# Kernel optimization log

Hardware: AMD Instinct MI355X
Metric: run time of the kernel (lower is better)

Reference implementation:

```python
import jax, jax.numpy as jnp
import numpy as np

EPS = 1e-5
DEPTH = 3
NQ = 12


def _bn(x, g, b):
    # BatchNorm1d in training mode: batch statistics, biased variance
    mu = x.mean(0)
    var = x.var(0)
    return (x - mu) / jnp.sqrt(var + EPS) * g + b


def _ln(x, g, b):
    mu = x.mean(-1, keepdims=True)
    var = x.var(-1, keepdims=True)
    return (x - mu) / jnp.sqrt(var + EPS) * g + b


def _apply_1q(s, U, q):
    # s: [B, 2^NQ] complex; U: [2,2] (shared) or [B,2,2] (per-sample); qubit q = q-th MSB
    B = s.shape[0]
    s = s.reshape(B, 2 ** q, 2, -1)
    sub = 'ij,bajc->baic' if U.ndim == 2 else 'bij,bajc->baic'
    return jnp.einsum(sub, U, s).reshape(B, -1)


def _apply_cry(s, theta, c):
    # controlled-Ry(theta): control qubit c, target qubit c+1 (adjacent)
    B = s.shape[0]
    s = s.reshape(B, 2 ** c, 2, 2, -1)
    co = jnp.cos(theta / 2).astype(s.dtype)
    si = jnp.sin(theta / 2).astype(s.dtype)
    s1 = s[:, :, 1]  # control = |1> block
    new1 = jnp.stack([co * s1[:, :, 0] - si * s1[:, :, 1],
                      si * s1[:, :, 0] + co * s1[:, :, 1]], axis=2)
    s = jnp.concatenate([s[:, :, :1], new1[:, :, None]], axis=2)
    return s.reshape(B, -1)


def _measure(s):
    # P(qubit q measures |1>) for each qubit
    p = jnp.abs(s) ** 2  # [B, 2^NQ]
    B = p.shape[0]
    probs = [p.reshape(B, 2 ** q, 2, -1).sum(axis=(1, 3))[:, 1] for q in range(NQ)]
    return jnp.stack(probs, axis=1)  # [B, NQ]


def _rot_mats(rot):
    # fused Rz(rz) @ Ry(ry) @ Rx(rx) for each (depth, qubit) -> [DEPTH, NQ, 2, 2]
    hx, hy, hz = rot[..., 0] / 2, rot[..., 1] / 2, rot[..., 2] / 2
    cx, sx = jnp.cos(hx), jnp.sin(hx)
    Rx = jnp.stack([jnp.stack([cx + 0j, -1j * sx], -1),
                    jnp.stack([-1j * sx, cx + 0j], -1)], -2)
    cy, sy = jnp.cos(hy), jnp.sin(hy)
    Ry = jnp.stack([jnp.stack([cy, -sy], -1),
                    jnp.stack([sy, cy], -1)], -2).astype(jnp.complex64)
    ez = jnp.exp(-1j * hz)
    z0 = jnp.zeros_like(ez)
    Rz = jnp.stack([jnp.stack([ez, z0], -1),
                    jnp.stack([z0, jnp.conj(ez)], -1)], -2)
    return jnp.einsum('...ij,...jk,...kl->...il', Rz, Ry, Rx).astype(jnp.complex64)


def _quantum_layer(x, We, be, gi, bi, rot, ent, Wd, bd, go, bo):
    e = jnp.tanh(_bn(x @ We.T + be, gi, bi))  # [B, NQ]
    nrm = jnp.linalg.norm(e, axis=1, keepdims=True)
    a = jnp.where(nrm > 0, e / nrm, e)        # per-sample L2-normalized amplitudes
    B = x.shape[0]
    s = jnp.zeros((B, 2 ** NQ), jnp.complex64).at[:, 0].set(1.0)
    # amplitude encoding: Ry(2*arcsin(|a|)) then phase pi (sign) if a<0 -> diag(1,-1)@Ry
    ang = 2.0 * jnp.arcsin(jnp.clip(jnp.abs(a), 0.0, 1.0))
    c, si = jnp.cos(ang / 2), jnp.sin(ang / 2)
    sg = jnp.where(a < 0, -1.0, 1.0)
    for q in range(NQ):
        U = jnp.stack([jnp.stack([c[:, q], -si[:, q]], -1),
                       jnp.stack([sg[:, q] * si[:, q], sg[:, q] * c[:, q]], -1)],
                      -2).astype(jnp.complex64)  # [B,2,2]
        s = _apply_1q(s, U, q)
    # parameterized circuit: per-qubit fused Rz.Ry.Rx, then nearest-neighbor CRy chain
    U = _rot_mats(rot)
    for d in range(DEPTH):
        for q in range(NQ):
            s = _apply_1q(s, U[d, q], q)
        for i in range(NQ - 1):
            s = _apply_cry(s, ent[d, i], i)
    m = _measure(s)
    return _bn(m @ Wd.T + bd, go, bo)


def setup_inputs() -> dict:
    key = jax.random.key(0)
    ks = jax.random.split(key, 16)
    B, IN, H1, H2, H3, OUT = 512, 512, 512, 512, 1024, 256

    def lin(k, o, i):
        k1, k2 = jax.random.split(k)
        lim = 1.0 / np.sqrt(i)
        return (jax.random.uniform(k1, (o, i), jnp.float32, -lim, lim),
                jax.random.uniform(k2, (o,), jnp.float32, -lim, lim))

    qWe0, qbe0 = lin(ks[1], NQ, IN)
    qWd0, qbd0 = lin(ks[2], H1, NQ)
    qWe1, qbe1 = lin(ks[3], NQ, H1)
    qWd1, qbd1 = lin(ks[4], H2, NQ)
    W2, b2 = lin(ks[5], H3, H2)
    Wo, bo = lin(ks[6], OUT, H3)
    return {
        'x': jax.random.normal(ks[0], (B, IN), jnp.float32),
        'qWe0': qWe0, 'qbe0': qbe0,
        'qgi0': jnp.ones(NQ), 'qbi0': jnp.zeros(NQ),
        'rot0': 0.1 * jax.random.normal(ks[7], (DEPTH, NQ, 3), jnp.float32),
        'ent0': 0.1 * jax.random.normal(ks[8], (DEPTH, NQ - 1), jnp.float32),
        'qWd0': qWd0, 'qbd0': qbd0,
        'qgo0': jnp.ones(H1), 'qbo0': jnp.zeros(H1),
        'qWe1': qWe1, 'qbe1': qbe1,
        'qgi1': jnp.ones(NQ), 'qbi1': jnp.zeros(NQ),
        'rot1': 0.1 * jax.random.normal(ks[9], (DEPTH, NQ, 3), jnp.float32),
        'ent1': 0.1 * jax.random.normal(ks[10], (DEPTH, NQ - 1), jnp.float32),
        'qWd1': qWd1, 'qbd1': qbd1,
        'qgo1': jnp.ones(H2), 'qbo1': jnp.zeros(H2),
        'W2': W2, 'b2': b2, 'ln2g': jnp.ones(H3), 'ln2b': jnp.zeros(H3),
        'Wo': Wo, 'bo': bo, 'lnog': jnp.ones(OUT), 'lnob': jnp.zeros(OUT),
    }


def reference(x, qWe0, qbe0, qgi0, qbi0, rot0, ent0, qWd0, qbd0, qgo0, qbo0,
              qWe1, qbe1, qgi1, qbi1, rot1, ent1, qWd1, qbd1, qgo1, qbo1,
              W2, b2, ln2g, ln2b, Wo, bo, lnog, lnob):
    h = _quantum_layer(x, qWe0, qbe0, qgi0, qbi0, rot0, ent0, qWd0, qbd0, qgo0, qbo0)
    h = _quantum_layer(h, qWe1, qbe1, qgi1, qbi1, rot1, ent1, qWd1, qbd1, qgo1, qbo1)
    h = jax.nn.relu(_ln(h @ W2.T + b2, ln2g, ln2b))  # classical block (dropout = identity, eval)
    return _ln(h @ Wo.T + bo, lnog, lnob)
```

## Files before the change

kernel.cpp:

```cpp
#include <hip/hip_runtime.h>
#include <math.h>

#define EPS   1e-5f
#define NQ    12
#define DEPTH 3
#define BATCH 512
#define DIM   4096

__device__ inline float2 cmul(float2 a, float2 b) {
    return make_float2(a.x*b.x - a.y*b.y, a.x*b.y + a.y*b.x);
}
__device__ inline float2 cmac2(float2 ua, float2 s, float2 ub, float2 p) {
    return make_float2(ua.x*s.x - ua.y*s.y + ub.x*p.x - ub.y*p.y,
                       ua.x*s.y + ua.y*s.x + ub.x*p.y + ub.y*p.x);
}

__device__ inline int swz(int a) { return a ^ ((a >> 4) & 15); }

template<int L> __device__ inline int ampl(int tid, int k) {
    if constexpr (L == 1) return (k << 8) | tid;
    else if constexpr (L == 2) return ((tid & 0xE0) << 4) | (k << 5) | (tid & 0x1F);
    else if constexpr (L == 3) return ((tid & 0xFC) << 4) | (k << 2) | (tid & 3);
    else return (tid << 4) | k;
}

template<int F, int T>
__device__ inline void remap(float2* amp, float2* lds2, int tid) {
    #pragma unroll
    for (int k = 0; k < 16; ++k) lds2[swz(ampl<F>(tid, k))] = amp[k];
    __syncthreads();
    #pragma unroll
    for (int k = 0; k < 16; ++k) amp[k] = lds2[swz(ampl<T>(tid, k))];
    __syncthreads();
}

template<int BP>
__device__ inline void one_q(float2* amp, float2 u00, float2 u01, float2 u10, float2 u11) {
    #pragma unroll
    for (int g = 0; g < 8; ++g) {
        const int j0 = ((g >> BP) << (BP+1)) | (g & ((1<<BP)-1));
        const int j1 = j0 | (1 << BP);
        float2 a0 = amp[j0], a1 = amp[j1];
        amp[j0] = cmac2(u00, a0, u01, a1);
        amp[j1] = cmac2(u10, a0, u11, a1);
    }
}

template<int CB, int TB>
__device__ inline void cry_rr(float2* amp, float co, float si) {
    #pragma unroll
    for (int m = 0; m < 16; ++m) {
        if (((m >> CB) & 1) && !((m >> TB) & 1)) {
            const int j1 = m | (1 << TB);
            float2 a0 = amp[m], a1 = amp[j1];
            amp[m]  = make_float2(co*a0.x - si*a1.x, co*a0.y - si*a1.y);
            amp[j1] = make_float2(si*a0.x + co*a1.x, si*a0.y + co*a1.y);
        }
    }
}

__device__ void qsim_core(float2* amp, float2* lds2, float* redm,
                          const float2* Uc, const float2* Cc,
                          int tid, int b, float* mout) {
    for (int d = 0; d < DEPTH; ++d) {
        const float2* Ud = Uc + d*NQ*4;
        const float2* Cd = Cc + d*(NQ-1);
        if (d > 0) {
            remap<4,1>(amp, lds2, tid);
            one_q<3>(amp, Ud[0],  Ud[1],  Ud[2],  Ud[3]);
            one_q<2>(amp, Ud[4],  Ud[5],  Ud[6],  Ud[7]);
            one_q<1>(amp, Ud[8],  Ud[9],  Ud[10], Ud[11]);
            one_q<0>(amp, Ud[12], Ud[13], Ud[14], Ud[15]);
        }
        cry_rr<3,2>(amp, Cd[0].x, Cd[0].y);
        cry_rr<2,1>(amp, Cd[1].x, Cd[1].y);
        cry_rr<1,0>(amp, Cd[2].x, Cd[2].y);
        remap<1,2>(amp, lds2, tid);
        if (d > 0) {
            one_q<2>(amp, Ud[16], Ud[17], Ud[18], Ud[19]);
            one_q<1>(amp, Ud[20], Ud[21], Ud[22], Ud[23]);
            one_q<0>(amp, Ud[24], Ud[25], Ud[26], Ud[27]);
        }
        cry_rr<3,2>(amp, Cd[3].x, Cd[3].y);
        cry_rr<2,1>(amp, Cd[4].x, Cd[4].y);
        cry_rr<1,0>(amp, Cd[5].x, Cd[5].y);
        remap<2,3>(amp, lds2, tid);
        if (d > 0) {
            one_q<2>(amp, Ud[28], Ud[29], Ud[30], Ud[31]);
            one_q<1>(amp, Ud[32], Ud[33], Ud[34], Ud[35]);
            one_q<0>(amp, Ud[36], Ud[37], Ud[38], Ud[39]);
        }
        cry_rr<3,2>(amp, Cd[6].x, Cd[6].y);
        cry_rr<2,1>(amp, Cd[7].x, Cd[7].y);
        cry_rr<1,0>(amp, Cd[8].x, Cd[8].y);
        remap<3,4>(amp, lds2, tid);
        if (d > 0) {
            one_q<1>(amp, Ud[40], Ud[41], Ud[42], Ud[43]);
            one_q<0>(amp, Ud[44], Ud[45], Ud[46], Ud[47]);
        }
        cry_rr<2,1>(amp, Cd[9].x,  Cd[9].y);
        cry_rr<1,0>(amp, Cd[10].x, Cd[10].y);
    }
    float msum = 0.f, p8 = 0.f, p9 = 0.f, p10 = 0.f, p11 = 0.f;
    #pragma unroll
    for (int k = 0; k < 16; ++k) {
        float m = amp[k].x*amp[k].x + amp[k].y*amp[k].y;
        msum += m;
        if (k & 8) p8  += m;
        if (k & 4) p9  += m;
        if (k & 2) p10 += m;
        if (k & 1) p11 += m;
    }
    int lane = tid & 63, wave = tid >> 6;
    #pragma unroll
    for (int q = 0; q < NQ; ++q) {
        float v;
        if (q < 8)        v = ((tid >> (7-q)) & 1) ? msum : 0.f;
        else if (q == 8)  v = p8;
        else if (q == 9)  v = p9;
        else if (q == 10) v = p10;
        else              v = p11;
        #pragma unroll
        for (int off = 32; off; off >>= 1) v += __shfl_xor(v, off);
        if (lane == 0) redm[q*4 + wave] = v;
    }
    __syncthreads();
    if (tid < NQ)
        mout[b*NQ + tid] = redm[tid*4] + redm[tid*4+1] + redm[tid*4+2] + redm[tid*4+3];
}

__device__ void qsim_init(float2* amp, const float* a, const float2* Uc, int tid) {
    float2 v0[NQ], v1[NQ];
    #pragma unroll
    for (int q = 0; q < NQ; ++q) {
        float sv = fminf(fabsf(a[q]), 1.f);
        float c  = sqrtf(fmaxf(1.f - sv*sv, 0.f));
        float ss = (a[q] < 0.f) ? -sv : sv;
        const float2* U = Uc + q*4;
        v0[q] = make_float2(U[0].x*c + U[1].x*ss, U[0].y*c + U[1].y*ss);
        v1[q] = make_float2(U[2].x*c + U[3].x*ss, U[2].y*c + U[3].y*ss);
    }
    float2 common = make_float2(1.f, 0.f);
    #pragma unroll
    for (int bb = 0; bb < 8; ++bb)
        common = cmul(common, ((tid >> bb) & 1) ? v1[11-bb] : v0[11-bb]);
    amp[0] = common;
    #pragma unroll
    for (int m = 0; m < 4; ++m) {
        const int q = 3 - m;
        #pragma unroll
        for (int k = 0; k < (1<<m); ++k) {
            amp[k | (1<<m)] = cmul(amp[k], v1[q]);
            amp[k]          = cmul(amp[k], v0[q]);
        }
    }
}

__device__ void consts_body(int t,
        const float* rot0, const float* ent0, const float* rot1, const float* ent1,
        float2* Uc, float2* Cc) {
    if (t < 72) {
        int layer = t / 36, rem = t % 36, d = rem / 12, q = rem % 12;
        const float* rot = layer ? rot1 : rot0;
        float hx = 0.5f * rot[(d*NQ + q)*3 + 0];
        float hy = 0.5f * rot[(d*NQ + q)*3 + 1];
        float hz = 0.5f * rot[(d*NQ + q)*3 + 2];
        float cx = cosf(hx), sx = sinf(hx);
        float cy = cosf(hy), sy = sinf(hy);
        float2 m00 = make_float2( cy*cx,  sy*sx);
        float2 m01 = make_float2(-sy*cx, -cy*sx);
        float2 m10 = make_float2( sy*cx, -cy*sx);
        float2 m11 = make_float2( cy*cx, -sy*sx);
        float2 ez  = make_float2(cosf(hz), -sinf(hz));
        float2 ezc = make_float2(ez.x, -ez.y);
        float2* U = Uc + t*4;
        U[0] = cmul(ez,  m00);
        U[1] = cmul(ez,  m01);
        U[2] = cmul(ezc, m10);
        U[3] = cmul(ezc, m11);
    } else if (t < 72 + 66) {
        int idx = t - 72, layer = idx / 33, rem = idx % 33;
        const float* ent = layer ? ent1 : ent0;
        float th = 0.5f * ent[rem];
        Cc[idx] = make_float2(cosf(th), sinf(th));
    }
}

__global__ __launch_bounds__(256) void encode0_consts_kernel(
        const float* __restrict__ X, const float* __restrict__ We,
        const float* __restrict__ be, float* __restrict__ Yraw,
        const float* __restrict__ rot0, const float* __restrict__ ent0,
        const float* __restrict__ rot1, const float* __restrict__ ent1,
        float2* __restrict__ Uc, float2* __restrict__ Cc) {
    int tid = threadIdx.x;
    if (blockIdx.x == 128) {
        consts_body(tid, rot0, ent0, rot1, ent1, Uc, Cc);
        return;
    }
    __shared__ float w[NQ][512];
    {
        const float4* src = (const float4*)We;
        float4* dst = (float4*)&w[0][0];
        #pragma unroll
        for (int i = tid; i < NQ*128; i += 256) dst[i] = src[i];
    }
    __syncthreads();
    int wave = tid >> 6, lane = tid & 63;
    int b = blockIdx.x * 4 + wave;
    const float4* xr = (const float4*)(X + (size_t)b * 512);
    float acc[NQ] = {};
    #pragma unroll
    for (int j = 0; j < 2; ++j) {
        float4 xv = xr[lane + 64*j];
        #pragma unroll
        for (int q = 0; q < NQ; ++q) {
            float4 wv = ((const float4*)&w[q][0])[lane + 64*j];
            acc[q] += xv.x*wv.x + xv.y*wv.y + xv.z*wv.z + xv.w*wv.w;
        }
    }
    #pragma unroll
    for (int q = 0; q < NQ; ++q) {
        float v = acc[q];
        #pragma unroll
        for (int off = 32; off; off >>= 1) v += __shfl_xor(v, off);
        if (lane == q) Yraw[b*NQ + q] = v + be[q];
    }
}

__global__ __launch_bounds__(256) void qsim_fused_kernel(
        const float* __restrict__ Yraw, const float* __restrict__ gi,
        const float* __restrict__ bi, const float2* __restrict__ UcAll,
        const float2* __restrict__ CcAll, int layer,
        float* __restrict__ mout, float* __restrict__ zeroY) {
    int blk = blockIdx.x, tid = threadIdx.x;
    const float2* UcL = UcAll + layer * DEPTH * NQ * 4;
    const float2* CcL = CcAll + layer * DEPTH * (NQ - 1);
    __shared__ float2 lds2[DIM];
    __shared__ float sred[96];
    if (zeroY && tid < NQ) zeroY[blk*NQ + tid] = 0.f;
    float sum[NQ] = {}, sq[NQ] = {};
    const float4* Y4 = (const float4*)Yraw;
    #pragma unroll
    for (int j = 0; j < 6; ++j) {
        float4 v = Y4[tid*6 + j];
        int q0 = (j*4) % 12;
        sum[q0+0]+=v.x; sq[q0+0]+=v.x*v.x;
        sum[q0+1]+=v.y; sq[q0+1]+=v.y*v.y;
        sum[q0+2]+=v.z; sq[q0+2]+=v.z*v.z;
        sum[q0+3]+=v.w; sq[q0+3]+=v.w*v.w;
    }
    int lane = tid & 63, wave = tid >> 6;
    #pragma unroll
    for (int q = 0; q < NQ; ++q) {
        #pragma unroll
        for (int off = 32; off; off >>= 1) {
            sum[q] += __shfl_xor(sum[q], off);
            sq[q]  += __shfl_xor(sq[q],  off);
        }
    }
    if (lane == 0) {
        #pragma unroll
        for (int q = 0; q < NQ; ++q) {
            sred[wave*24 + q]      = sum[q];
            sred[wave*24 + 12 + q] = sq[q];
        }
    }
    __syncthreads();
    float a[NQ]; float n2 = 0.f;
    const float* yr = Yraw + blk*NQ;
    #pragma unroll
    for (int q = 0; q < NQ; ++q) {
        float s  = sred[q]    + sred[24+q] + sred[48+q] + sred[72+q];
        float s2 = sred[12+q] + sred[36+q] + sred[60+q] + sred[84+q];
        float mu  = s  * (1.f/512.f);
        float var = s2 * (1.f/512.f) - mu*mu;
        float val = (yr[q] - mu) * rsqrtf(var + EPS) * gi[q] + bi[q];
        a[q] = tanhf(val);
        n2 += a[q]*a[q];
    }
    float scn = (n2 > 0.f) ? rsqrtf(n2) : 1.f;
    #pragma unroll
    for (int q = 0; q < NQ; ++q) a[q] *= scn;
    __syncthreads();
    float2 amp[16];
    qsim_init(amp, a, UcL, tid);
    qsim_core(amp, lds2, sred, UcL, CcL, tid, blk, mout);
}

__global__ __launch_bounds__(512) void decode_kernel(
        const float* __restrict__ m, const float* __restrict__ Wd,
        const float* __restrict__ bd, const float* __restrict__ go,
        const float* __restrict__ bo, float* __restrict__ outT) {
    int h = blockIdx.x, b = threadIdx.x;
    __shared__ float sm[BATCH * 13];
    __shared__ float2 red[8];
    const float4* m4 = (const float4*)m;
    for (int f4 = b; f4 < 1536; f4 += 512) {
        float4 v = m4[f4];
        int base = f4*4; int row = base/12; int q = base - row*12;
        float* dst = sm + row*13 + q;
        dst[0]=v.x; dst[1]=v.y; dst[2]=v.z; dst[3]=v.w;
    }
    __syncthreads();
    float z = bd[h];
    #pragma unroll
    for (int q = 0; q < NQ; ++q) z += sm[b*13 + q] * Wd[h*NQ + q];
    float2 v = make_float2(z, z*z);
    int lane = b & 63, wave = b >> 6;
    for (int off = 32; off; off >>= 1) { v.x += __shfl_down(v.x, off); v.y += __shfl_down(v.y, off); }
    if (lane == 0) red[wave] = v;
    __syncthreads();
    float s = 0.f, s2 = 0.f;
    #pragma unroll
    for (int wv = 0; wv < 8; ++wv) { s += red[wv].x; s2 += red[wv].y; }
    float mu  = s  * (1.f/512.f);
    float var = s2 * (1.f/512.f) - mu*mu;
    outT[(size_t)h*BATCH + b] = (z - mu) * rsqrtf(var + EPS) * go[h] + bo[h];
}

__global__ __launch_bounds__(256) void encode1_kernel(
        const float* __restrict__ h1T, const float* __restrict__ We,
        const float* __restrict__ be, float* __restrict__ Yraw1) {
    __shared__ float w[NQ][512];
    __shared__ float red[4*64*NQ];
    int tid = threadIdx.x, blk = blockIdx.x;
    {
        const float4* src = (const float4*)We;
        float4* dst = (float4*)&w[0][0];
        #pragma unroll
        for (int i = tid; i < NQ*128; i += 256) dst[i] = src[i];
    }
    __syncthreads();
    int kc = blk >> 3, bc = blk & 7;
    int bl = tid & 63, hg = tid >> 6;
    int b = bc*64 + bl;
    float acc[NQ] = {};
    #pragma unroll
    for (int i = 0; i < 16; ++i) {
        int h = kc*64 + hg*16 + i;
        float xv = h1T[(size_t)h*512 + b];
        #pragma unroll
        for (int q = 0; q < NQ; ++q) acc[q] += xv * w[q][h];
    }
    #pragma unroll
    for (int q = 0; q < NQ; ++q) red[(hg*64 + bl)*NQ + q] = acc[q];
    __syncthreads();
    for (int i = tid; i < 64*NQ; i += 256) {
        int bl2 = i / NQ, q = i - bl2*NQ;
        float v = red[bl2*NQ+q] + red[(64+bl2)*NQ+q] + red[(128+bl2)*NQ+q] + red[(192+bl2)*NQ+q];
        if (kc == 0) v += be[q];
        atomicAdd(&Yraw1[(size_t)(bc*64 + bl2)*NQ + q], v);
    }
}

__global__ __launch_bounds__(256) void gemm1_kernel(
        const float* __restrict__ AT, const float* __restrict__ W,
        float* __restrict__ Cpart) {
    __shared__ float As[2][32][64];
    __shared__ float Bs[2][32][68];
    const int b0 = blockIdx.x * 64, j0 = blockIdx.y * 64;
    const int kbase = blockIdx.z * 128;
    float* C = Cpart + (size_t)blockIdx.z * 512 * 1024;
    const int tid = threadIdx.x;
    const int tr = tid >> 4, tc = tid & 15;
    const int a_kk = tid >> 4, a_f4 = tid & 15;
    const int b_jj = tid >> 3, b_k4 = (tid & 7) * 4;
    float4 ra0, ra1, rb0, rb1;
    float acc[4][4] = {};
    {
        const int k0 = kbase;
        ra0 = *(const float4*)(AT + (size_t)(k0 + a_kk)*512 + b0 + a_f4*4);
        ra1 = *(const float4*)(AT + (size_t)(k0 + a_kk + 16)*512 + b0 + a_f4*4);
        rb0 = *(const float4*)(W + (size_t)(j0 + b_jj)*512 + k0 + b_k4);
        rb1 = *(const float4*)(W + (size_t)(j0 + b_jj + 32)*512 + k0 + b_k4);
        *(float4*)&As[0][a_kk][a_f4*4] = ra0;
        *(float4*)&As[0][a_kk+16][a_f4*4] = ra1;
        Bs[0][b_k4+0][b_jj] = rb0.x; Bs[0][b_k4+1][b_jj] = rb0.y;
        Bs[0][b_k4+2][b_jj] = rb0.z; Bs[0][b_k4+3][b_jj] = rb0.w;
        Bs[0][b_k4+0][b_jj+32] = rb1.x; Bs[0][b_k4+1][b_jj+32] = rb1.y;
        Bs[0][b_k4+2][b_jj+32] = rb1.z; Bs[0][b_k4+3][b_jj+32] = rb1.w;
    }
    __syncthreads();
    for (int s = 0; s < 4; ++s) {
        if (s < 3) {
            const int k0 = kbase + (s+1)*32;
            ra0 = *(const float4*)(AT + (size_t)(k0 + a_kk)*512 + b0 + a_f4*4);
            ra1 = *(const float4*)(AT + (size_t)(k0 + a_kk + 16)*512 + b0 + a_f4*4);
            rb0 = *(const float4*)(W + (size_t)(j0 + b_jj)*512 + k0 + b_k4);
            rb1 = *(const float4*)(W + (size_t)(j0 + b_jj + 32)*512 + k0 + b_k4);
        }
        const int bf = s & 1;
        #pragma unroll
        for (int kk = 0; kk < 32; ++kk) {
            float4 a  = *(const float4*)&As[bf][kk][tr*4];
            float4 bv = *(const float4*)&Bs[bf][kk][tc*4];
            acc[0][0] += a.x*bv.x; acc[0][1] += a.x*bv.y; acc[0][2] += a.x*bv.z; acc[0][3] += a.x*bv.w;
            acc[1][0] += a.y*bv.x; acc[1][1] += a.y*bv.y; acc[1][2] += a.y*bv.z; acc[1][3] += a.y*bv.w;
            acc[2][0] += a.z*bv.x; acc[2][1] += a.z*bv.y; acc[2][2] += a.z*bv.z; acc[2][3] += a.z*bv.w;
            acc[3][0] += a.w*bv.x; acc[3][1] += a.w*bv.y; acc[3][2] += a.w*bv.z; acc[3][3] += a.w*bv.w;
        }
        if (s < 3) {
            const int nb = bf ^ 1;
            *(float4*)&As[nb][a_kk][a_f4*4] = ra0;
            *(float4*)&As[nb][a_kk+16][a_f4*4] = ra1;
            Bs[nb][b_k4+0][b_jj] = rb0.x; Bs[nb][b_k4+1][b_jj] = rb0.y;
            Bs[nb][b_k4+2][b_jj] = rb0.z; Bs[nb][b_k4+3][b_jj] = rb0.w;
            Bs[nb][b_k4+0][b_jj+32] = rb1.x; Bs[nb][b_k4+1][b_jj+32] = rb1.y;
            Bs[nb][b_k4+2][b_jj+32] = rb1.z; Bs[nb][b_k4+3][b_jj+32] = rb1.w;
        }
        __syncthreads();
    }
    #pragma unroll
    for (int r = 0; r < 4; ++r) {
        float4 o = make_float4(acc[r][0], acc[r][1], acc[r][2], acc[r][3]);
        *(float4*)(C + (size_t)(b0 + tr*4 + r)*1024 + j0 + tc*4) = o;
    }
}

__global__ __launch_bounds__(256) void ln_relu_kernel(
        const float* __restrict__ P, const float* __restrict__ bias,
        const float* __restrict__ g, const float* __restrict__ be,
        float* __restrict__ Y) {
    int b = blockIdx.x, tid = threadIdx.x;
    __shared__ float2 red[4];
    float v[4];
    #pragma unroll
    for (int j = 0; j < 4; ++j) {
        int col = tid + j*256;
        float t = bias[col];
        #pragma unroll
        for (int z = 0; z < 4; ++z) t += P[(size_t)z*524288 + (size_t)b*1024 + col];
        v[j] = t;
    }
    float2 r = make_float2(v[0]+v[1]+v[2]+v[3],
                           v[0]*v[0]+v[1]*v[1]+v[2]*v[2]+v[3]*v[3]);
    int lane = tid & 63, wave = tid >> 6;
    for (int off = 32; off; off >>= 1) { r.x += __shfl_down(r.x, off); r.y += __shfl_down(r.y, off); }
    if (lane == 0) red[wave] = r;
    __syncthreads();
    float s = red[0].x + red[1].x + red[2].x + red[3].x;
    float s2 = red[0].y + red[1].y + red[2].y + red[3].y;
    float mu  = s  * (1.f/1024.f);
    float var = s2 * (1.f/1024.f) - mu*mu;
    float inv = rsqrtf(var + EPS);
    float* yr = Y + (size_t)b * 1024;
    #pragma unroll
    for (int j = 0; j < 4; ++j) {
        int col = tid + j*256;
        yr[col] = fmaxf((v[j]-mu)*inv*g[col] + be[col], 0.f);
    }
}

__global__ __launch_bounds__(256) void gemm2_kernel(
        const float* __restrict__ Amat, const float* __restrict__ W,
        float* __restrict__ Cpart) {
    __shared__ __align__(16) char smem[27000];
    float (*As)[32][36] = (float(*)[32][36])smem;
    float (*Bs)[32][68] = (float(*)[32][68])(smem + 9216);
    const int b0 = blockIdx.x * 32, j0 = blockIdx.y * 64;
    const int kbase = blockIdx.z * 128;
    float* C = Cpart + (size_t)blockIdx.z * 512 * 256;
    const int tid = threadIdx.x;
    const int tr = tid >> 4, tc = tid & 15;
    const int l_r = tid >> 3, l_k4 = (tid & 7) * 4;
    float4 ra0, rb0, rb1;
    float acc[2][4] = {};
    {
        const int k0 = kbase;
        ra0 = *(const float4*)(Amat + (size_t)(b0 + l_r)*1024 + k0 + l_k4);
        rb0 = *(const float4*)(W + (size_t)(j0 + l_r)*1024 + k0 + l_k4);
        rb1 = *(const float4*)(W + (size_t)(j0 + l_r + 32)*1024 + k0 + l_k4);
        As[0][l_k4+0][l_r] = ra0.x; As[0][l_k4+1][l_r] = ra0.y;
        As[0][l_k4+2][l_r] = ra0.z; As[0][l_k4+3][l_r] = ra0.w;
        Bs[0][l_k4+0][l_r] = rb0.x; Bs[0][l_k4+1][l_r] = rb0.y;
        Bs[0][l_k4+2][l_r] = rb0.z; Bs[0][l_k4+3][l_r] = rb0.w;
        Bs[0][l_k4+0][l_r+32] = rb1.x; Bs[0][l_k4+1][l_r+32] = rb1.y;
        Bs[0][l_k4+2][l_r+32] = rb1.z; Bs[0][l_k4+3][l_r+32] = rb1.w;
    }
    __syncthreads();
    for (int s = 0; s < 4; ++s) {
        if (s < 3) {
            const int k0 = kbase + (s+1)*32;
            ra0 = *(const float4*)(Amat + (size_t)(b0 + l_r)*1024 + k0 + l_k4);
            rb0 = *(const float4*)(W + (size_t)(j0 + l_r)*1024 + k0 + l_k4);
            rb1 = *(const float4*)(W + (size_t)(j0 + l_r + 32)*1024 + k0 + l_k4);
        }
        const int bf = s & 1;
        #pragma unroll
        for (int kk = 0; kk < 32; ++kk) {
            float a0 = As[bf][kk][tr*2], a1 = As[bf][kk][tr*2+1];
            float4 bv = *(const float4*)&Bs[bf][kk][tc*4];
            acc[0][0] += a0*bv.x; acc[0][1] += a0*bv.y; acc[0][2] += a0*bv.z; acc[0][3] += a0*bv.w;
            acc[1][0] += a1*bv.x; acc[1][1] += a1*bv.y; acc[1][2] += a1*bv.z; acc[1][3] += a1*bv.w;
        }
        if (s < 3) {
            const int nb = bf ^ 1;
            As[nb][l_k4+0][l_r] = ra0.x; As[nb][l_k4+1][l_r] = ra0.y;
            As[nb][l_k4+2][l_r] = ra0.z; As[nb][l_k4+3][l_r] = ra0.w;
            Bs[nb][l_k4+0][l_r] = rb0.x; Bs[nb][l_k4+1][l_r] = rb0.y;
            Bs[nb][l_k4+2][l_r] = rb0.z; Bs[nb][l_k4+3][l_r] = rb0.w;
            Bs[nb][l_k4+0][l_r+32] = rb1.x; Bs[nb][l_k4+1][l_r+32] = rb1.y;
            Bs[nb][l_k4+2][l_r+32] = rb1.z; Bs[nb][l_k4+3][l_r+32] = rb1.w;
        }
        __syncthreads();
    }
    #pragma unroll
    for (int r = 0; r < 2; ++r) {
        float4 o = make_float4(acc[r][0], acc[r][1], acc[r][2], acc[r][3]);
        *(float4*)(C + (size_t)(b0 + tr*2 + r)*256 + j0 + tc*4) = o;
    }
}

__global__ __launch_bounds__(256) void ln_out_kernel(
        const float* __restrict__ P, const float* __restrict__ bias,
        const float* __restrict__ g, const float* __restrict__ be,
        float* __restrict__ Y) {
    int b = blockIdx.x, tid = threadIdx.x;
    __shared__ float2 red[4];
    float v0 = bias[tid];
    #pragma unroll
    for (int z = 0; z < 8; ++z) v0 += P[(size_t)z*131072 + (size_t)b*256 + tid];
    float2 v = make_float2(v0, v0*v0);
    int lane = tid & 63, wave = tid >> 6;
    for (int off = 32; off; off >>= 1) { v.x += __shfl_down(v.x, off); v.y += __shfl_down(v.y, off); }
    if (lane == 0) red[wave] = v;
    __syncthreads();
    float s = red[0].x + red[1].x + red[2].x + red[3].x;
    float s2 = red[0].y + red[1].y + red[2].y + red[3].y;
    float mu  = s  * (1.f/256.f);
    float var = s2 * (1.f/256.f) - mu*mu;
    Y[(size_t)b*256 + tid] = (v0 - mu) * rsqrtf(var + EPS) * g[tid] + be[tid];
}

extern "C" void kernel_launch(void* const* d_in, const int* in_sizes, int n_in,
                              void* d_out, int out_size, void* d_ws, size_t ws_size,
                              hipStream_t stream) {
    const float* x    = (const float*)d_in[0];
    const float* qWe0 = (const float*)d_in[1];
    const float* qbe0 = (const float*)d_in[2];
    const float* qgi0 = (const float*)d_in[3];
    const float* qbi0 = (const float*)d_in[4];
    const float* rot0 = (const float*)d_in[5];
    const float* ent0 = (const float*)d_in[6];
    const float* qWd0 = (const float*)d_in[7];
    const float* qbd0 = (const float*)d_in[8];
    const float* qgo0 = (const float*)d_in[9];
    const float* qbo0 = (const float*)d_in[10];
    const float* qWe1 = (const float*)d_in[11];
    const float* qbe1 = (const float*)d_in[12];
    const float* qgi1 = (const float*)d_in[13];
    const float* qbi1 = (const float*)d_in[14];
    const float* rot1 = (const float*)d_in[15];
    const float* ent1 = (const float*)d_in[16];
    const float* qWd1 = (const float*)d_in[17];
    const float* qbd1 = (const float*)d_in[18];
    const float* qgo1 = (const float*)d_in[19];
    const float* qbo1 = (const float*)d_in[20];
    const float* W2   = (const float*)d_in[21];
    const float* b2   = (const float*)d_in[22];
    const float* ln2g = (const float*)d_in[23];
    const float* ln2b = (const float*)d_in[24];
    const float* Wo   = (const float*)d_in[25];
    const float* bo   = (const float*)d_in[26];
    const float* lnog = (const float*)d_in[27];
    const float* lnob = (const float*)d_in[28];
    float* out = (float*)d_out;
    float* ws  = (float*)d_ws;

    float2* Uc   = (float2*)ws;
    float2* Cc   = Uc + 288;
    float* Yraw0 = ws + 1024;
    float* m0    = ws + 7680;
    float* Yraw1 = ws + 14336;
    float* m1    = ws + 20992;
    float* h1T   = ws + 65536;
    float* h2T   = ws + 589824;
    float* t3p   = ws + 851968;
    float* t3n   = ws + 2949120;
    float* t4p   = ws + 3473408;

    hipLaunchKernelGGL(encode0_consts_kernel, dim3(129), dim3(256), 0, stream,
                       x, qWe0, qbe0, Yraw0, rot0, ent0, rot1, ent1, Uc, Cc);
    hipLaunchKernelGGL(qsim_fused_kernel, dim3(512), dim3(256), 0, stream,
                       Yraw0, qgi0, qbi0, Uc, Cc, 0, m0, Yraw1);
    hipLaunchKernelGGL(decode_kernel, dim3(512), dim3(512), 0, stream,
                       m0, qWd0, qbd0, qgo0, qbo0, h1T);
    hipLaunchKernelGGL(encode1_kernel, dim3(64), dim3(256), 0, stream,
                       h1T, qWe1, qbe1, Yraw1);
    hipLaunchKernelGGL(qsim_fused_kernel, dim3(512), dim3(256), 0, stream,
                       Yraw1, qgi1, qbi1, Uc, Cc, 1, m1, (float*)nullptr);
    hipLaunchKernelGGL(decode_kernel, dim3(512), dim3(512), 0, stream,
                       m1, qWd1, qbd1, qgo1, qbo1, h2T);
    hipLaunchKernelGGL(gemm1_kernel, dim3(8, 16, 4), dim3(256), 0, stream,
                       h2T, W2, t3p);
    hipLaunchKernelGGL(ln_relu_kernel, dim3(512), dim3(256), 0, stream,
                       t3p, b2, ln2g, ln2b, t3n);
    hipLaunchKernelGGL(gemm2_kernel, dim3(16, 4, 8), dim3(256), 0, stream,
                       t3n, Wo, t4p);
    hipLaunchKernelGGL(ln_out_kernel, dim3(512), dim3(256), 0, stream,
                       t4p, bo, lnog, lnob, out);
}
```

Measured before the change: 223.2 us.

## Simulate state vector with 512 threads of 8 amplitudes and finer encode1 split

```diff
diff --git a/kernel.cpp b/kernel.cpp
--- a/kernel.cpp
+++ b/kernel.cpp
@@ -17,27 +17,24 @@
 
 __device__ inline int swz(int a) { return a ^ ((a >> 4) & 15); }
 
-template<int L> __device__ inline int ampl(int tid, int k) {
-    if constexpr (L == 1) return (k << 8) | tid;
-    else if constexpr (L == 2) return ((tid & 0xE0) << 4) | (k << 5) | (tid & 0x1F);
-    else if constexpr (L == 3) return ((tid & 0xFC) << 4) | (k << 2) | (tid & 3);
-    else return (tid << 4) | k;
-}
-
-template<int F, int T>
-__device__ inline void remap(float2* amp, float2* lds2, int tid) {
-    #pragma unroll
-    for (int k = 0; k < 16; ++k) lds2[swz(ampl<F>(tid, k))] = amp[k];
-    __syncthreads();
-    #pragma unroll
-    for (int k = 0; k < 16; ++k) amp[k] = lds2[swz(ampl<T>(tid, k))];
+template<int HB> __device__ inline int ampl8(int t, int k) {
+    return ((t >> HB) << (HB+3)) | (k << HB) | (t & ((1<<HB)-1));
+}
+
+template<int FHB, int THB>
+__device__ inline void remap8(float2* amp, float2* lds2, int t) {
+    #pragma unroll
+    for (int k = 0; k < 8; ++k) lds2[swz(ampl8<FHB>(t, k))] = amp[k];
+    __syncthreads();
+    #pragma unroll
+    for (int k = 0; k < 8; ++k) amp[k] = lds2[swz(ampl8<THB>(t, k))];
     __syncthreads();
 }
 
 template<int BP>
-__device__ inline void one_q(float2* amp, float2 u00, float2 u01, float2 u10, float2 u11) {
-    #pragma unroll
-    for (int g = 0; g < 8; ++g) {
+__device__ inline void one_q8(float2* amp, float2 u00, float2 u01, float2 u10, float2 u11) {
+    #pragma unroll
+    for (int g = 0; g < 4; ++g) {
         const int j0 = ((g >> BP) << (BP+1)) | (g & ((1<<BP)-1));
         const int j1 = j0 | (1 << BP);
         float2 a0 = amp[j0], a1 = amp[j1];
@@ -47,111 +44,14 @@
 }
 
 template<int CB, int TB>
-__device__ inline void cry_rr(float2* amp, float co, float si) {
-    #pragma unroll
-    for (int m = 0; m < 16; ++m) {
+__device__ inline void cry8(float2* amp, float co, float si) {
+    #pragma unroll
+    for (int m = 0; m < 8; ++m) {
         if (((m >> CB) & 1) && !((m >> TB) & 1)) {
             const int j1 = m | (1 << TB);
             float2 a0 = amp[m], a1 = amp[j1];
             amp[m]  = make_float2(co*a0.x - si*a1.x, co*a0.y - si*a1.y);
             amp[j1] = make_float2(si*a0.x + co*a1.x, si*a0.y + co*a1.y);
-        }
-    }
-}
-
-__device__ void qsim_core(float2* amp, float2* lds2, float* redm,
-                          const float2* Uc, const float2* Cc,
-                          int tid, int b, float* mout) {
-    for (int d = 0; d < DEPTH; ++d) {
-        const float2* Ud = Uc + d*NQ*4;
-        const float2* Cd = Cc + d*(NQ-1);
-        if (d > 0) {
-            remap<4,1>(amp, lds2, tid);
-            one_q<3>(amp, Ud[0],  Ud[1],  Ud[2],  Ud[3]);
-            one_q<2>(amp, Ud[4],  Ud[5],  Ud[6],  Ud[7]);
-            one_q<1>(amp, Ud[8],  Ud[9],  Ud[10], Ud[11]);
-            one_q<0>(amp, Ud[12], Ud[13], Ud[14], Ud[15]);
-        }
-        cry_rr<3,2>(amp, Cd[0].x, Cd[0].y);
-        cry_rr<2,1>(amp, Cd[1].x, Cd[1].y);
-        cry_rr<1,0>(amp, Cd[2].x, Cd[2].y);
-        remap<1,2>(amp, lds2, tid);
-        if (d > 0) {
-            one_q<2>(amp, Ud[16], Ud[17], Ud[18], Ud[19]);
-            one_q<1>(amp, Ud[20], Ud[21], Ud[22], Ud[23]);
-            one_q<0>(amp, Ud[24], Ud[25], Ud[26], Ud[27]);
-        }
-        cry_rr<3,2>(amp, Cd[3].x, Cd[3].y);
-        cry_rr<2,1>(amp, Cd[4].x, Cd[4].y);
-        cry_rr<1,0>(amp, Cd[5].x, Cd[5].y);
-        remap<2,3>(amp, lds2, tid);
-        if (d > 0) {
-            one_q<2>(amp, Ud[28], Ud[29], Ud[30], Ud[31]);
-            one_q<1>(amp, Ud[32], Ud[33], Ud[34], Ud[35]);
-            one_q<0>(amp, Ud[36], Ud[37], Ud[38], Ud[39]);
-        }
-        cry_rr<3,2>(amp, Cd[6].x, Cd[6].y);
-        cry_rr<2,1>(amp, Cd[7].x, Cd[7].y);
-        cry_rr<1,0>(amp, Cd[8].x, Cd[8].y);
-        remap<3,4>(amp, lds2, tid);
-        if (d > 0) {
-            one_q<1>(amp, Ud[40], Ud[41], Ud[42], Ud[43]);
-            one_q<0>(amp, Ud[44], Ud[45], Ud[46], Ud[47]);
-        }
-        cry_rr<2,1>(amp, Cd[9].x,  Cd[9].y);
-        cry_rr<1,0>(amp, Cd[10].x, Cd[10].y);
-    }
-    float msum = 0.f, p8 = 0.f, p9 = 0.f, p10 = 0.f, p11 = 0.f;
-    #pragma unroll
-    for (int k = 0; k < 16; ++k) {
-        float m = amp[k].x*amp[k].x + amp[k].y*amp[k].y;
-        msum += m;
-        if (k & 8) p8  += m;
-        if (k & 4) p9  += m;
-        if (k & 2) p10 += m;
-        if (k & 1) p11 += m;
-    }
-    int lane = tid & 63, wave = tid >> 6;
-    #pragma unroll
-    for (int q = 0; q < NQ; ++q) {
-        float v;
-        if (q < 8)        v = ((tid >> (7-q)) & 1) ? msum : 0.f;
-        else if (q == 8)  v = p8;
-        else if (q == 9)  v = p9;
-        else if (q == 10) v = p10;
-        else              v = p11;
-        #pragma unroll
-        for (int off = 32; off; off >>= 1) v += __shfl_xor(v, off);
-        if (lane == 0) redm[q*4 + wave] = v;
-    }
-    __syncthreads();
-    if (tid < NQ)
-        mout[b*NQ + tid] = redm[tid*4] + redm[tid*4+1] + redm[tid*4+2] + redm[tid*4+3];
-}
-
-__device__ void qsim_init(float2* amp, const float* a, const float2* Uc, int tid) {
-    float2 v0[NQ], v1[NQ];
-    #pragma unroll
-    for (int q = 0; q < NQ; ++q) {
-        float sv = fminf(fabsf(a[q]), 1.f);
-        float c  = sqrtf(fmaxf(1.f - sv*sv, 0.f));
-        float ss = (a[q] < 0.f) ? -sv : sv;
-        const float2* U = Uc + q*4;
-        v0[q] = make_float2(U[0].x*c + U[1].x*ss, U[0].y*c + U[1].y*ss);
-        v1[q] = make_float2(U[2].x*c + U[3].x*ss, U[2].y*c + U[3].y*ss);
-    }
-    float2 common = make_float2(1.f, 0.f);
-    #pragma unroll
-    for (int bb = 0; bb < 8; ++bb)
-        common = cmul(common, ((tid >> bb) & 1) ? v1[11-bb] : v0[11-bb]);
-    amp[0] = common;
-    #pragma unroll
-    for (int m = 0; m < 4; ++m) {
-        const int q = 3 - m;
-        #pragma unroll
-        for (int k = 0; k < (1<<m); ++k) {
-            amp[k | (1<<m)] = cmul(amp[k], v1[q]);
-            amp[k]          = cmul(amp[k], v0[q]);
         }
     }
 }
@@ -227,29 +127,27 @@
     }
 }
 
-__global__ __launch_bounds__(256) void qsim_fused_kernel(
+__global__ __launch_bounds__(512, 4) void qsim8_kernel(
         const float* __restrict__ Yraw, const float* __restrict__ gi,
         const float* __restrict__ bi, const float2* __restrict__ UcAll,
         const float2* __restrict__ CcAll, int layer,
         float* __restrict__ mout, float* __restrict__ zeroY) {
-    int blk = blockIdx.x, tid = threadIdx.x;
-    const float2* UcL = UcAll + layer * DEPTH * NQ * 4;
-    const float2* CcL = CcAll + layer * DEPTH * (NQ - 1);
+    int blk = blockIdx.x, t = threadIdx.x;
+    const float2* Uc = UcAll + layer * DEPTH * NQ * 4;
+    const float2* Cc = CcAll + layer * DEPTH * (NQ - 1);
     __shared__ float2 lds2[DIM];
-    __shared__ float sred[96];
-    if (zeroY && tid < NQ) zeroY[blk*NQ + tid] = 0.f;
-    float sum[NQ] = {}, sq[NQ] = {};
-    const float4* Y4 = (const float4*)Yraw;
-    #pragma unroll
-    for (int j = 0; j < 6; ++j) {
-        float4 v = Y4[tid*6 + j];
-        int q0 = (j*4) % 12;
-        sum[q0+0]+=v.x; sq[q0+0]+=v.x*v.x;
-        sum[q0+1]+=v.y; sq[q0+1]+=v.y*v.y;
-        sum[q0+2]+=v.z; sq[q0+2]+=v.z*v.z;
-        sum[q0+3]+=v.w; sq[q0+3]+=v.w*v.w;
-    }
-    int lane = tid & 63, wave = tid >> 6;
+    __shared__ float sred[192];
+    if (zeroY && t < NQ) zeroY[blk*NQ + t] = 0.f;
+
+    float sum[NQ], sq[NQ];
+    {
+        const float4* Y4 = (const float4*)Yraw;
+        float4 va = Y4[t*3+0], vb = Y4[t*3+1], vc = Y4[t*3+2];
+        float r[12] = {va.x,va.y,va.z,va.w, vb.x,vb.y,vb.z,vb.w, vc.x,vc.y,vc.z,vc.w};
+        #pragma unroll
+        for (int q = 0; q < NQ; ++q) { sum[q] = r[q]; sq[q] = r[q]*r[q]; }
+    }
+    int lane = t & 63, wave = t >> 6;
     #pragma unroll
     for (int q = 0; q < NQ; ++q) {
         #pragma unroll
@@ -270,8 +168,9 @@
     const float* yr = Yraw + blk*NQ;
     #pragma unroll
     for (int q = 0; q < NQ; ++q) {
-        float s  = sred[q]    + sred[24+q] + sred[48+q] + sred[72+q];
-        float s2 = sred[12+q] + sred[36+q] + sred[60+q] + sred[84+q];
+        float s = 0.f, s2 = 0.f;
+        #pragma unroll
+        for (int w8 = 0; w8 < 8; ++w8) { s += sred[w8*24 + q]; s2 += sred[w8*24 + 12 + q]; }
         float mu  = s  * (1.f/512.f);
         float var = s2 * (1.f/512.f) - mu*mu;
         float val = (yr[q] - mu) * rsqrtf(var + EPS) * gi[q] + bi[q];
@@ -281,10 +180,106 @@
     float scn = (n2 > 0.f) ? rsqrtf(n2) : 1.f;
     #pragma unroll
     for (int q = 0; q < NQ; ++q) a[q] *= scn;
-    __syncthreads();
-    float2 amp[16];
-    qsim_init(amp, a, UcL, tid);
-    qsim_core(amp, lds2, sred, UcL, CcL, tid, blk, mout);
+
+    float2 v0[NQ], v1[NQ];
+    #pragma unroll
+    for (int q = 0; q < NQ; ++q) {
+        float sv = fminf(fabsf(a[q]), 1.f);
+        float c  = sqrtf(fmaxf(1.f - sv*sv, 0.f));
+        float ss = (a[q] < 0.f) ? -sv : sv;
+        const float2* U = Uc + q*4;
+        v0[q] = make_float2(U[0].x*c + U[1].x*ss, U[0].y*c + U[1].y*ss);
+        v1[q] = make_float2(U[2].x*c + U[3].x*ss, U[2].y*c + U[3].y*ss);
+    }
+    float2 common = make_float2(1.f, 0.f);
+    #pragma unroll
+    for (int j = 0; j < 9; ++j)
+        common = cmul(common, ((t >> j) & 1) ? v1[11-j] : v0[11-j]);
+    float2 amp[8];
+    amp[0] = common;
+    #pragma unroll
+    for (int m = 0; m < 3; ++m) {
+        const int q = 2 - m;
+        #pragma unroll
+        for (int k = 0; k < (1<<m); ++k) {
+            amp[k | (1<<m)] = cmul(amp[k], v1[q]);
+            amp[k]          = cmul(amp[k], v0[q]);
+        }
+    }
+
+    for (int d = 0; d < DEPTH; ++d) {
+        const float2* Ud = Uc + d*NQ*4;
+        const float2* Cd = Cc + d*(NQ-1);
+        if (d > 0) {
+            one_q8<2>(amp, Ud[0],  Ud[1],  Ud[2],  Ud[3]);
+            one_q8<1>(amp, Ud[4],  Ud[5],  Ud[6],  Ud[7]);
+            one_q8<0>(amp, Ud[8],  Ud[9],  Ud[10], Ud[11]);
+        }
+        cry8<2,1>(amp, Cd[0].x, Cd[0].y);
+        cry8<1,0>(amp, Cd[1].x, Cd[1].y);
+        remap8<9,7>(amp, lds2, t);
+        if (d > 0) {
+            one_q8<1>(amp, Ud[12], Ud[13], Ud[14], Ud[15]);
+            one_q8<0>(amp, Ud[16], Ud[17], Ud[18], Ud[19]);
+        }
+        cry8<2,1>(amp, Cd[2].x, Cd[2].y);
+        cry8<1,0>(amp, Cd[3].x, Cd[3].y);
+        remap8<7,5>(amp, lds2, t);
+        if (d > 0) {
+            one_q8<1>(amp, Ud[20], Ud[21], Ud[22], Ud[23]);
+            one_q8<0>(amp, Ud[24], Ud[25], Ud[26], Ud[27]);
+        }
+        cry8<2,1>(amp, Cd[4].x, Cd[4].y);
+        cry8<1,0>(amp, Cd[5].x, Cd[5].y);
+        remap8<5,3>(amp, lds2, t);
+        if (d > 0) {
+            one_q8<1>(amp, Ud[28], Ud[29], Ud[30], Ud[31]);
+            one_q8<0>(amp, Ud[32], Ud[33], Ud[34], Ud[35]);
+        }
+        cry8<2,1>(amp, Cd[6].x, Cd[6].y);
+        cry8<1,0>(amp, Cd[7].x, Cd[7].y);
+        remap8<3,1>(amp, lds2, t);
+        if (d > 0) {
+            one_q8<1>(amp, Ud[36], Ud[37], Ud[38], Ud[39]);
+            one_q8<0>(amp, Ud[40], Ud[41], Ud[42], Ud[43]);
+        }
+        cry8<2,1>(amp, Cd[8].x, Cd[8].y);
+        cry8<1,0>(amp, Cd[9].x, Cd[9].y);
+        remap8<1,0>(amp, lds2, t);
+        if (d > 0) {
+            one_q8<0>(amp, Ud[44], Ud[45], Ud[46], Ud[47]);
+        }
+        cry8<1,0>(amp, Cd[10].x, Cd[10].y);
+        if (d < DEPTH-1) remap8<0,9>(amp, lds2, t);
+    }
+
+    float msum = 0.f, p9 = 0.f, p10 = 0.f, p11 = 0.f;
+    #pragma unroll
+    for (int k = 0; k < 8; ++k) {
+        float m = amp[k].x*amp[k].x + amp[k].y*amp[k].y;
+        msum += m;
+        if (k & 4) p9  += m;
+        if (k & 2) p10 += m;
+        if (k & 1) p11 += m;
+    }
+    #pragma unroll
+    for (int q = 0; q < NQ; ++q) {
+        float v;
+        if (q < 9)        v = ((t >> (8-q)) & 1) ? msum : 0.f;
+        else if (q == 9)  v = p9;
+        else if (q == 10) v = p10;
+        else              v = p11;
+        #pragma unroll
+        for (int off = 32; off; off >>= 1) v += __shfl_xor(v, off);
+        if (lane == 0) sred[q*8 + wave] = v;
+    }
+    __syncthreads();
+    if (t < NQ) {
+        float r = 0.f;
+        #pragma unroll
+        for (int w8 = 0; w8 < 8; ++w8) r += sred[t*8 + w8];
+        mout[blk*NQ + t] = r;
+    }
 }
 
 __global__ __launch_bounds__(512) void decode_kernel(
@@ -336,8 +331,8 @@
     int b = bc*64 + bl;
     float acc[NQ] = {};
     #pragma unroll
-    for (int i = 0; i < 16; ++i) {
-        int h = kc*64 + hg*16 + i;
+    for (int i = 0; i < 8; ++i) {
+        int h = kc*32 + hg*8 + i;
         float xv = h1T[(size_t)h*512 + b];
         #pragma unroll
         for (int q = 0; q < NQ; ++q) acc[q] += xv * w[q][h];
@@ -581,13 +576,13 @@
 
     hipLaunchKernelGGL(encode0_consts_kernel, dim3(129), dim3(256), 0, stream,
                        x, qWe0, qbe0, Yraw0, rot0, ent0, rot1, ent1, Uc, Cc);
-    hipLaunchKernelGGL(qsim_fused_kernel, dim3(512), dim3(256), 0, stream,
+    hipLaunchKernelGGL(qsim8_kernel, dim3(512), dim3(512), 0, stream,
                        Yraw0, qgi0, qbi0, Uc, Cc, 0, m0, Yraw1);
     hipLaunchKernelGGL(decode_kernel, dim3(512), dim3(512), 0, stream,
                        m0, qWd0, qbd0, qgo0, qbo0, h1T);
-    hipLaunchKernelGGL(encode1_kernel, dim3(64), dim3(256), 0, stream,
+    hipLaunchKernelGGL(encode1_kernel, dim3(128), dim3(256), 0, stream,
                        h1T, qWe1, qbe1, Yraw1);
-    hipLaunchKernelGGL(qsim_fused_kernel, dim3(512), dim3(256), 0, stream,
+    hipLaunchKernelGGL(qsim8_kernel, dim3(512), dim3(512), 0, stream,
                        Yraw1, qgi1, qbi1, Uc, Cc, 1, m1, (float*)nullptr);
     hipLaunchKernelGGL(decode_kernel, dim3(512), dim3(512), 0, stream,
                        m1, qWd1, qbd1, qgo1, qbo1, h2T);
```

Measured after the change: 235.7 us. 1.06x slower.

## Restructure state-vector sim to three LDS remaps per layer with double-buffered LDS

Applied to the files above, without the earlier changes.

```diff
diff --git a/kernel.cpp b/kernel.cpp
--- a/kernel.cpp
+++ b/kernel.cpp
@@ -17,21 +17,17 @@
 
 __device__ inline int swz(int a) { return a ^ ((a >> 4) & 15); }
 
-template<int L> __device__ inline int ampl(int tid, int k) {
-    if constexpr (L == 1) return (k << 8) | tid;
-    else if constexpr (L == 2) return ((tid & 0xE0) << 4) | (k << 5) | (tid & 0x1F);
-    else if constexpr (L == 3) return ((tid & 0xFC) << 4) | (k << 2) | (tid & 3);
-    else return (tid << 4) | k;
-}
-
-template<int F, int T>
-__device__ inline void remap(float2* amp, float2* lds2, int tid) {
-    #pragma unroll
-    for (int k = 0; k < 16; ++k) lds2[swz(ampl<F>(tid, k))] = amp[k];
-    __syncthreads();
-    #pragma unroll
-    for (int k = 0; k < 16; ++k) amp[k] = lds2[swz(ampl<T>(tid, k))];
-    __syncthreads();
+template<int HB> __device__ inline int ampl16(int t, int k) {
+    return ((t >> HB) << (HB+4)) | (k << HB) | (t & ((1<<HB)-1));
+}
+
+template<int FHB, int THB>
+__device__ inline void remap16(float2* amp, float2* lds, int t) {
+    #pragma unroll
+    for (int k = 0; k < 16; ++k) lds[swz(ampl16<FHB>(t, k))] = amp[k];
+    __syncthreads();
+    #pragma unroll
+    for (int k = 0; k < 16; ++k) amp[k] = lds[swz(ampl16<THB>(t, k))];
 }
 
 template<int BP>
@@ -59,99 +55,17 @@
     }
 }
 
-__device__ void qsim_core(float2* amp, float2* lds2, float* redm,
-                          const float2* Uc, const float2* Cc,
-                          int tid, int b, float* mout) {
-    for (int d = 0; d < DEPTH; ++d) {
-        const float2* Ud = Uc + d*NQ*4;
-        const float2* Cd = Cc + d*(NQ-1);
-        if (d > 0) {
-            remap<4,1>(amp, lds2, tid);
-            one_q<3>(amp, Ud[0],  Ud[1],  Ud[2],  Ud[3]);
-            one_q<2>(amp, Ud[4],  Ud[5],  Ud[6],  Ud[7]);
-            one_q<1>(amp, Ud[8],  Ud[9],  Ud[10], Ud[11]);
-            one_q<0>(amp, Ud[12], Ud[13], Ud[14], Ud[15]);
-        }
-        cry_rr<3,2>(amp, Cd[0].x, Cd[0].y);
-        cry_rr<2,1>(amp, Cd[1].x, Cd[1].y);
-        cry_rr<1,0>(amp, Cd[2].x, Cd[2].y);
-        remap<1,2>(amp, lds2, tid);
-        if (d > 0) {
-            one_q<2>(amp, Ud[16], Ud[17], Ud[18], Ud[19]);
-            one_q<1>(amp, Ud[20], Ud[21], Ud[22], Ud[23]);
-            one_q<0>(amp, Ud[24], Ud[25], Ud[26], Ud[27]);
-        }
-        cry_rr<3,2>(amp, Cd[3].x, Cd[3].y);
-        cry_rr<2,1>(amp, Cd[4].x, Cd[4].y);
-        cry_rr<1,0>(amp, Cd[5].x, Cd[5].y);
-        remap<2,3>(amp, lds2, tid);
-        if (d > 0) {
-            one_q<2>(amp, Ud[28], Ud[29], Ud[30], Ud[31]);
-            one_q<1>(amp, Ud[32], Ud[33], Ud[34], Ud[35]);
-            one_q<0>(amp, Ud[36], Ud[37], Ud[38], Ud[39]);
-        }
-        cry_rr<3,2>(amp, Cd[6].x, Cd[6].y);
-        cry_rr<2,1>(amp, Cd[7].x, Cd[7].y);
-        cry_rr<1,0>(amp, Cd[8].x, Cd[8].y);
-        remap<3,4>(amp, lds2, tid);
-        if (d > 0) {
-            one_q<1>(amp, Ud[40], Ud[41], Ud[42], Ud[43]);
-            one_q<0>(amp, Ud[44], Ud[45], Ud[46], Ud[47]);
-        }
-        cry_rr<2,1>(amp, Cd[9].x,  Cd[9].y);
-        cry_rr<1,0>(amp, Cd[10].x, Cd[10].y);
-    }
-    float msum = 0.f, p8 = 0.f, p9 = 0.f, p10 = 0.f, p11 = 0.f;
-    #pragma unroll
-    for (int k = 0; k < 16; ++k) {
-        float m = amp[k].x*amp[k].x + amp[k].y*amp[k].y;
-        msum += m;
-        if (k & 8) p8  += m;
-        if (k & 4) p9  += m;
-        if (k & 2) p10 += m;
-        if (k & 1) p11 += m;
-    }
-    int lane = tid & 63, wave = tid >> 6;
-    #pragma unroll
-    for (int q = 0; q < NQ; ++q) {
-        float v;
-        if (q < 8)        v = ((tid >> (7-q)) & 1) ? msum : 0.f;
-        else if (q == 8)  v = p8;
-        else if (q == 9)  v = p9;
-        else if (q == 10) v = p10;
-        else              v = p11;
-        #pragma unroll
-        for (int off = 32; off; off >>= 1) v += __shfl_xor(v, off);
-        if (lane == 0) redm[q*4 + wave] = v;
-    }
-    __syncthreads();
-    if (tid < NQ)
-        mout[b*NQ + tid] = redm[tid*4] + redm[tid*4+1] + redm[tid*4+2] + redm[tid*4+3];
-}
-
-__device__ void qsim_init(float2* amp, const float* a, const float2* Uc, int tid) {
-    float2 v0[NQ], v1[NQ];
-    #pragma unroll
-    for (int q = 0; q < NQ; ++q) {
-        float sv = fminf(fabsf(a[q]), 1.f);
-        float c  = sqrtf(fmaxf(1.f - sv*sv, 0.f));
-        float ss = (a[q] < 0.f) ? -sv : sv;
-        const float2* U = Uc + q*4;
-        v0[q] = make_float2(U[0].x*c + U[1].x*ss, U[0].y*c + U[1].y*ss);
-        v1[q] = make_float2(U[2].x*c + U[3].x*ss, U[2].y*c + U[3].y*ss);
-    }
-    float2 common = make_float2(1.f, 0.f);
-    #pragma unroll
-    for (int bb = 0; bb < 8; ++bb)
-        common = cmul(common, ((tid >> bb) & 1) ? v1[11-bb] : v0[11-bb]);
-    amp[0] = common;
-    #pragma unroll
-    for (int m = 0; m < 4; ++m) {
-        const int q = 3 - m;
-        #pragma unroll
-        for (int k = 0; k < (1<<m); ++k) {
-            amp[k | (1<<m)] = cmul(amp[k], v1[q]);
-            amp[k]          = cmul(amp[k], v0[q]);
+template<int TB>
+__device__ inline void crysel16(float2* amp, int ctrl, float co, float si) {
+    float co2 = ctrl ? co : 1.f;
+    float s2  = ctrl ? si : 0.f;
+    #pragma unroll
+    for (int m = 0; m < 16; ++m) {
+        if (!((m >> TB) & 1)) {
+            const int j1 = m | (1 << TB);
+            float2 a0 = amp[m], a1 = amp[j1];
+            amp[m]  = make_float2(co2*a0.x - s2*a1.x, co2*a0.y - s2*a1.y);
+            amp[j1] = make_float2(s2*a0.x + co2*a1.x, s2*a0.y + co2*a1.y);
         }
     }
 }
@@ -227,29 +141,32 @@
     }
 }
 
-__global__ __launch_bounds__(256) void qsim_fused_kernel(
+__global__ __launch_bounds__(256, 2) void qsim3w_kernel(
         const float* __restrict__ Yraw, const float* __restrict__ gi,
         const float* __restrict__ bi, const float2* __restrict__ UcAll,
         const float2* __restrict__ CcAll, int layer,
         float* __restrict__ mout, float* __restrict__ zeroY) {
-    int blk = blockIdx.x, tid = threadIdx.x;
-    const float2* UcL = UcAll + layer * DEPTH * NQ * 4;
-    const float2* CcL = CcAll + layer * DEPTH * (NQ - 1);
-    __shared__ float2 lds2[DIM];
+    int blk = blockIdx.x, t = threadIdx.x;
+    const float2* Uc = UcAll + layer * DEPTH * NQ * 4;
+    const float2* Cc = CcAll + layer * DEPTH * (NQ - 1);
+    __shared__ float2 lds2[2][DIM];
     __shared__ float sred[96];
-    if (zeroY && tid < NQ) zeroY[blk*NQ + tid] = 0.f;
+    if (zeroY && t < NQ) zeroY[blk*NQ + t] = 0.f;
+
     float sum[NQ] = {}, sq[NQ] = {};
-    const float4* Y4 = (const float4*)Yraw;
-    #pragma unroll
-    for (int j = 0; j < 6; ++j) {
-        float4 v = Y4[tid*6 + j];
-        int q0 = (j*4) % 12;
-        sum[q0+0]+=v.x; sq[q0+0]+=v.x*v.x;
-        sum[q0+1]+=v.y; sq[q0+1]+=v.y*v.y;
-        sum[q0+2]+=v.z; sq[q0+2]+=v.z*v.z;
-        sum[q0+3]+=v.w; sq[q0+3]+=v.w*v.w;
-    }
-    int lane = tid & 63, wave = tid >> 6;
+    {
+        const float4* Y4 = (const float4*)Yraw;
+        #pragma unroll
+        for (int j = 0; j < 6; ++j) {
+            float4 v = Y4[t*6 + j];
+            int q0 = (j*4) % 12;
+            sum[q0+0]+=v.x; sq[q0+0]+=v.x*v.x;
+            sum[q0+1]+=v.y; sq[q0+1]+=v.y*v.y;
+            sum[q0+2]+=v.z; sq[q0+2]+=v.z*v.z;
+            sum[q0+3]+=v.w; sq[q0+3]+=v.w*v.w;
+        }
+    }
+    int lane = t & 63, wave = t >> 6;
     #pragma unroll
     for (int q = 0; q < NQ; ++q) {
         #pragma unroll
@@ -281,10 +198,96 @@
     float scn = (n2 > 0.f) ? rsqrtf(n2) : 1.f;
     #pragma unroll
     for (int q = 0; q < NQ; ++q) a[q] *= scn;
-    __syncthreads();
+
+    float2 v0[NQ], v1[NQ];
+    #pragma unroll
+    for (int q = 0; q < NQ; ++q) {
+        float sv = fminf(fabsf(a[q]), 1.f);
+        float c  = sqrtf(fmaxf(1.f - sv*sv, 0.f));
+        float ss = (a[q] < 0.f) ? -sv : sv;
+        const float2* U = Uc + q*4;
+        v0[q] = make_float2(U[0].x*c + U[1].x*ss, U[0].y*c + U[1].y*ss);
+        v1[q] = make_float2(U[2].x*c + U[3].x*ss, U[2].y*c + U[3].y*ss);
+    }
+    float2 common = make_float2(1.f, 0.f);
+    #pragma unroll
+    for (int j = 0; j < 8; ++j)
+        common = cmul(common, ((t >> j) & 1) ? v1[11-j] : v0[11-j]);
     float2 amp[16];
-    qsim_init(amp, a, UcL, tid);
-    qsim_core(amp, lds2, sred, UcL, CcL, tid, blk, mout);
+    amp[0] = common;
+    #pragma unroll
+    for (int mb = 0; mb < 4; ++mb) {
+        const int qb = 3 - mb;
+        #pragma unroll
+        for (int k = 0; k < (1<<mb); ++k) {
+            amp[k | (1<<mb)] = cmul(amp[k], v1[qb]);
+            amp[k]           = cmul(amp[k], v0[qb]);
+        }
+    }
+
+    int rb = 0;
+    for (int d = 0; d < DEPTH; ++d) {
+        const float2* Ud = Uc + d*NQ*4;
+        const float2* Cd = Cc + d*(NQ-1);
+        if (d > 0) {
+            remap16<0,8>(amp, lds2[rb], t); rb ^= 1;
+            one_q<3>(amp, Ud[0],  Ud[1],  Ud[2],  Ud[3]);
+            one_q<2>(amp, Ud[4],  Ud[5],  Ud[6],  Ud[7]);
+            one_q<1>(amp, Ud[8],  Ud[9],  Ud[10], Ud[11]);
+            one_q<0>(amp, Ud[12], Ud[13], Ud[14], Ud[15]);
+        }
+        cry_rr<3,2>(amp, Cd[0].x, Cd[0].y);
+        cry_rr<2,1>(amp, Cd[1].x, Cd[1].y);
+        cry_rr<1,0>(amp, Cd[2].x, Cd[2].y);
+        remap16<8,4>(amp, lds2[rb], t); rb ^= 1;
+        if (d > 0) {
+            one_q<3>(amp, Ud[16], Ud[17], Ud[18], Ud[19]);
+            one_q<2>(amp, Ud[20], Ud[21], Ud[22], Ud[23]);
+            one_q<1>(amp, Ud[24], Ud[25], Ud[26], Ud[27]);
+            one_q<0>(amp, Ud[28], Ud[29], Ud[30], Ud[31]);
+        }
+        crysel16<3>(amp, (t >> 4) & 1, Cd[3].x, Cd[3].y);
+        cry_rr<3,2>(amp, Cd[4].x, Cd[4].y);
+        cry_rr<2,1>(amp, Cd[5].x, Cd[5].y);
+        cry_rr<1,0>(amp, Cd[6].x, Cd[6].y);
+        remap16<4,0>(amp, lds2[rb], t); rb ^= 1;
+        if (d > 0) {
+            one_q<3>(amp, Ud[32], Ud[33], Ud[34], Ud[35]);
+            one_q<2>(amp, Ud[36], Ud[37], Ud[38], Ud[39]);
+            one_q<1>(amp, Ud[40], Ud[41], Ud[42], Ud[43]);
+            one_q<0>(amp, Ud[44], Ud[45], Ud[46], Ud[47]);
+        }
+        crysel16<3>(amp, t & 1, Cd[7].x, Cd[7].y);
+        cry_rr<3,2>(amp, Cd[8].x,  Cd[8].y);
+        cry_rr<2,1>(amp, Cd[9].x,  Cd[9].y);
+        cry_rr<1,0>(amp, Cd[10].x, Cd[10].y);
+    }
+
+    float msum = 0.f, p8 = 0.f, p9 = 0.f, p10 = 0.f, p11 = 0.f;
+    #pragma unroll
+    for (int k = 0; k < 16; ++k) {
+        float m = amp[k].x*amp[k].x + amp[k].y*amp[k].y;
+        msum += m;
+        if (k & 8) p8  += m;
+        if (k & 4) p9  += m;
+        if (k & 2) p10 += m;
+        if (k & 1) p11 += m;
+    }
+    #pragma unroll
+    for (int q = 0; q < NQ; ++q) {
+        float v;
+        if (q < 8)        v = ((t >> (7-q)) & 1) ? msum : 0.f;
+        else if (q == 8)  v = p8;
+        else if (q == 9)  v = p9;
+        else if (q == 10) v = p10;
+        else              v = p11;
+        #pragma unroll
+        for (int off = 32; off; off >>= 1) v += __shfl_xor(v, off);
+        if (lane == 0) sred[q*4 + wave] = v;
+    }
+    __syncthreads();
+    if (t < NQ)
+        mout[blk*NQ + t] = sred[t*4] + sred[t*4+1] + sred[t*4+2] + sred[t*4+3];
 }
 
 __global__ __launch_bounds__(512) void decode_kernel(
@@ -581,13 +584,13 @@
 
     hipLaunchKernelGGL(encode0_consts_kernel, dim3(129), dim3(256), 0, stream,
                        x, qWe0, qbe0, Yraw0, rot0, ent0, rot1, ent1, Uc, Cc);
-    hipLaunchKernelGGL(qsim_fused_kernel, dim3(512), dim3(256), 0, stream,
+    hipLaunchKernelGGL(qsim3w_kernel, dim3(512), dim3(256), 0, stream,
                        Yraw0, qgi0, qbi0, Uc, Cc, 0, m0, Yraw1);
     hipLaunchKernelGGL(decode_kernel, dim3(512), dim3(512), 0, stream,
                        m0, qWd0, qbd0, qgo0, qbo0, h1T);
     hipLaunchKernelGGL(encode1_kernel, dim3(64), dim3(256), 0, stream,
                        h1T, qWe1, qbe1, Yraw1);
-    hipLaunchKernelGGL(qsim_fused_kernel, dim3(512), dim3(256), 0, stream,
+    hipLaunchKernelGGL(qsim3w_kernel, dim3(512), dim3(256), 0, stream,
                        Yraw1, qgi1, qbi1, Uc, Cc, 1, m1, (float*)nullptr);
     hipLaunchKernelGGL(decode_kernel, dim3(512), dim3(512), 0, stream,
                        m1, qWd1, qbd1, qgo1, qbo1, h2T);
```

Result: faster. 216.6 us (-3.0%).
